# Optimization experiments

Measured on AMD Instinct MI355X. Metric: run time of the kernel, lower is better.

The kernel has to match this reference:

```python
import jax, jax.numpy as jnp
import numpy as np

M = 8192          # tokens (batch*seq)
K = 4096          # in_features
N = 4096          # out_features
BK = 64           # block_k (row_block of B)
BN = 64           # block_n (col_block of B)
NR = K // BK      # 64 block rows of B
NC = N // BN      # 64 block cols of B
OCC = 4           # nonzero blocks per column (and per row)
TB = NR * OCC     # total nonzero blocks = 256


def _build_indices():
    # Regular block mask: each column has OCC nonzero block-rows, each row has OCC
    # nonzero block-cols (matches BlockMask.regular invariants). Deterministic
    # construction: column c uses rows (c + s*(NR//OCC)) % NR, sorted ascending.
    step = NR // OCC
    cols = np.arange(NC)
    rows = np.sort((cols[None, :] + step * np.arange(OCC)[:, None]) % NR, axis=0)  # [OCC, NC]
    # _build_data_indices assigns data slots column-major, row-ascending within a
    # column, so column c's blocks (sorted by row) get slots c*OCC + s.
    data = cols[None, :] * OCC + np.arange(OCC)[:, None]  # [OCC, NC]
    return rows.astype(np.int32), data.astype(np.int32)


def setup_inputs() -> dict:
    key = jax.random.key(0)
    k1, k2 = jax.random.split(key)
    rows, data = _build_indices()
    return {
        "A": jax.random.normal(k1, (M, K), dtype=jnp.float32),
        "B_data": jax.random.normal(k2, (BK, BN * TB), dtype=jnp.float32) * 0.02,
        "row_indices": jnp.asarray(rows),
        "data_indices": jnp.asarray(data),
    }


def reference(A, B_data, row_indices, data_indices):
    # A: [M, K]; B_data: [BK, BN*TB]; indices: [OCC, NC]
    m, k = A.shape
    occ, nc = row_indices.shape
    bk = B_data.shape[0]
    tb = occ * nc
    bn = B_data.shape[1] // tb
    nr = k // bk
    # Gather A blocks per (sub_k, out_col): [m, occ, nc, bk]
    A_blocks = A.reshape(m, nr, bk)[:, row_indices]
    # Gather B blocks: B_data laid out as [bk, tb, bn] -> [tb, bk, bn] -> [occ, nc, bk, bn]
    B_blocks = jnp.transpose(B_data.reshape(bk, tb, bn), (1, 0, 2))[data_indices]
    # Accumulate over occ and bk (fp32 accumulation like the Triton kernel)
    C = jnp.einsum('mock,ockn->mcn', A_blocks, B_blocks,
                   preferred_element_type=jnp.float32)
    return C.reshape(m, nc * bn).astype(A.dtype)
```

## Files before the change

### kernel.cpp

```cpp
#include <hip/hip_runtime.h>
#include <hip/hip_bf16.h>

typedef __bf16 bf16x8 __attribute__((ext_vector_type(8)));
typedef float  f32x4  __attribute__((ext_vector_type(4)));

__device__ __forceinline__ void dma16(const float* g, float* l) {
    typedef const __attribute__((address_space(1))) unsigned int* gp_t;
    typedef __attribute__((address_space(3))) unsigned int*       lp_t;
    __builtin_amdgcn_global_load_lds((gp_t)(const void*)g, (lp_t)(void*)l, 16, 0, 0);
}

__global__ __launch_bounds__(256, 2) void sparse_linear_kernel(
    const float* __restrict__ A, const float* __restrict__ Bd,
    const int* __restrict__ rowi, const int* __restrict__ di,
    float* __restrict__ C)
{
    __shared__ __align__(16) unsigned short Bt[4 * 64 * 64];
    __shared__ __align__(16) float Aring[4][3][16 * 64];
    char* BtB = (char*)Bt;

    const int bid = blockIdx.x;
    const int c   = bid & 63;
    const int mch = bid >> 6;
    const int t    = threadIdx.x;
    const int lane = t & 63;
    const int w    = t >> 6;

    int rs[4], ds[4];
    #pragma unroll
    for (int s = 0; s < 4; ++s) {
        rs[s] = rowi[s * 64 + c];
        ds[s] = di[s * 64 + c];
    }
    int koff[4];
    #pragma unroll
    for (int s = 0; s < 4; ++s) koff[s] = rs[s] * 64;

    const long mbase = (long)mch * 256 + w * 64;

    #pragma unroll
    for (int st = 0; st < 3; ++st) {
        float* slotp = &Aring[w][st][0];
        #pragma unroll
        for (int i = 0; i < 4; ++i) {
            const int rr  = i * 4 + (lane >> 4);
            const int kfl = (((lane & 15) * 16) ^ (rr << 4)) >> 2;
            const float* g = A + (mbase + st * 16 + rr) * 4096 + koff[0] + kfl;
            dma16(g, slotp + i * 256);
        }
    }

    {
        const int n  = t & 63;
        const int sb = t >> 6;
        const float* Bg = Bd + (long)ds[sb] * 64 + n;
        char* dst = BtB + sb * 8192 + n * 128;
        const int sw = (n & 7) << 4;
        #pragma unroll
        for (int k4 = 0; k4 < 16; ++k4) {
            union { ushort4 u; __bf16 e[4]; } pk;
            pk.e[0] = (__bf16)Bg[(long)(4 * k4 + 0) * 16384];
            pk.e[1] = (__bf16)Bg[(long)(4 * k4 + 1) * 16384];
            pk.e[2] = (__bf16)Bg[(long)(4 * k4 + 2) * 16384];
            pk.e[3] = (__bf16)Bg[(long)(4 * k4 + 3) * 16384];
            *(ushort4*)(dst + ((8 * k4) ^ sw)) = pk.u;
        }
    }
    __syncthreads();

    f32x4 acc[4][4];
    #pragma unroll
    for (int m = 0; m < 4; ++m)
        #pragma unroll
        for (int n2 = 0; n2 < 4; ++n2) acc[m][n2] = f32x4{0.f, 0.f, 0.f, 0.f};

    bf16x8 bfr[2][4];

    #pragma unroll
    for (int step = 0; step < 16; ++step) {
        const int s = step >> 2, mt = step & 3, slot = step % 3;

        if (step <= 13)      asm volatile("s_waitcnt vmcnt(8)" ::: "memory");
        else if (step == 14) asm volatile("s_waitcnt vmcnt(4)" ::: "memory");
        else                 asm volatile("s_waitcnt vmcnt(0)" ::: "memory");
        __builtin_amdgcn_sched_barrier(0);

        if (mt == 0) {
            const char* bbase = BtB + s * 8192;
            #pragma unroll
            for (int kh = 0; kh < 2; ++kh)
                #pragma unroll
                for (int n2 = 0; n2 < 4; ++n2) {
                    const int nr = n2 * 16 + (lane & 15);
                    const int kb = kh * 64 + (lane >> 4) * 16;
                    bfr[kh][n2] = *(const bf16x8*)(bbase + nr * 128 + (kb ^ ((nr & 7) << 4)));
                }
        }

        const char* ab = (const char*)&Aring[w][slot][0];
        const int r   = lane & 15;
        const int q32 = (lane >> 4) * 32;
        f32x4 a0 = *(const f32x4*)(ab + r * 256 + ((q32)            ^ (r << 4)));
        f32x4 a1 = *(const f32x4*)(ab + r * 256 + ((q32 + 16)       ^ (r << 4)));
        f32x4 a2 = *(const f32x4*)(ab + r * 256 + ((128 + q32)      ^ (r << 4)));
        f32x4 a3 = *(const f32x4*)(ab + r * 256 + ((128 + q32 + 16) ^ (r << 4)));
        union { bf16x8 v; __bf16 e[8]; } af0, af1;
        #pragma unroll
        for (int i = 0; i < 4; ++i) {
            af0.e[i]     = (__bf16)a0[i];
            af0.e[i + 4] = (__bf16)a1[i];
            af1.e[i]     = (__bf16)a2[i];
            af1.e[i + 4] = (__bf16)a3[i];
        }

        __builtin_amdgcn_s_setprio(1);
        #pragma unroll
        for (int kh = 0; kh < 2; ++kh) {
            const bf16x8 afv = kh ? af1.v : af0.v;
            #pragma unroll
            for (int n2 = 0; n2 < 4; ++n2)
                acc[mt][n2] = __builtin_amdgcn_mfma_f32_16x16x32_bf16(afv, bfr[kh][n2], acc[mt][n2], 0, 0, 0);
        }
        __builtin_amdgcn_s_setprio(0);

        if (step + 3 < 16) {
            const int s2 = (step + 3) >> 2, mt2 = (step + 3) & 3;
            float* slotp = &Aring[w][slot][0];
            #pragma unroll
            for (int i = 0; i < 4; ++i) {
                const int rr  = i * 4 + (lane >> 4);
                const int kfl = (((lane & 15) * 16) ^ (rr << 4)) >> 2;
                const float* g = A + (mbase + mt2 * 16 + rr) * 4096 + koff[s2] + kfl;
                dma16(g, slotp + i * 256);
            }
        }
    }

    #pragma unroll
    for (int mt = 0; mt < 4; ++mt) {
        const long crow0 = mbase + mt * 16 + (lane >> 4) * 4;
        const long col0  = (long)c * 64 + (lane & 15);
        #pragma unroll
        for (int n2 = 0; n2 < 4; ++n2)
            #pragma unroll
            for (int v = 0; v < 4; ++v)
                __builtin_nontemporal_store(acc[mt][n2][v],
                    &C[(crow0 + v) * 4096 + col0 + n2 * 16]);
    }
}

extern "C" void kernel_launch(void* const* d_in, const int* in_sizes, int n_in,
                              void* d_out, int out_size, void* d_ws, size_t ws_size,
                              hipStream_t stream) {
    const float* A    = (const float*)d_in[0];
    const float* Bd   = (const float*)d_in[1];
    const int*   rowi = (const int*)d_in[2];
    const int*   di   = (const int*)d_in[3];
    float*       C    = (float*)d_out;

    dim3 grid(32 * 64);
    dim3 block(256);
    hipLaunchKernelGGL(sparse_linear_kernel, grid, block, 0, stream,
                       A, Bd, rowi, di, C);
}
```

Baseline: 58.45 us.

## Process four M-chunks per block to reuse converted B tile, quarter grid

Each workgroup now handles four 256-row chunks of A for its output column block instead of one, so the B-block gather and bf16 conversion into LDS is amortised over four times more work and the grid shrinks from 2048 to 512 blocks. The A DMA ring runs continuously across chunk boundaries, and each chunk's results are written out and the accumulators reset before the next chunk begins. With 256 CUs and 2 blocks/CU this leaves exactly one wave of blocks, but it removes the tail-overlap benefit of more blocks. Store traffic issued mid-loop may interfere with the vmcnt-based waits. The final chunk also issues redundant clamped prefetches.

Measured after the change: 56.25 us. 3.8% less time.

```diff
diff --git a/kernel.cpp b/kernel.cpp
--- a/kernel.cpp
+++ b/kernel.cpp
@@ -15,13 +15,13 @@
     const int* __restrict__ rowi, const int* __restrict__ di,
     float* __restrict__ C)
 {
+    __shared__ __align__(16) float Aring[4][3][16 * 64];
     __shared__ __align__(16) unsigned short Bt[4 * 64 * 64];
-    __shared__ __align__(16) float Aring[4][3][16 * 64];
     char* BtB = (char*)Bt;
 
     const int bid = blockIdx.x;
     const int c   = bid & 63;
-    const int mch = bid >> 6;
+    const int grp = bid >> 6;
     const int t    = threadIdx.x;
     const int lane = t & 63;
     const int w    = t >> 6;
@@ -36,19 +36,22 @@
     #pragma unroll
     for (int s = 0; s < 4; ++s) koff[s] = rs[s] * 64;
 
-    const long mbase = (long)mch * 256 + w * 64;
+    const long wrow0 = (long)grp * 1024 + w * 64;
 
-    #pragma unroll
-    for (int st = 0; st < 3; ++st) {
-        float* slotp = &Aring[w][st][0];
+    auto dmaA = [&](int q, int kb, int mt, int slot) {
+        float* slotp = &Aring[w][slot][0];
         #pragma unroll
         for (int i = 0; i < 4; ++i) {
             const int rr  = i * 4 + (lane >> 4);
             const int kfl = (((lane & 15) * 16) ^ (rr << 4)) >> 2;
-            const float* g = A + (mbase + st * 16 + rr) * 4096 + koff[0] + kfl;
+            const float* g = A + (wrow0 + q * 256 + mt * 16 + rr) * 4096 + koff[kb] + kfl;
             dma16(g, slotp + i * 256);
         }
-    }
+    };
+
+    dmaA(0, 0, 0, 0);
+    dmaA(0, 0, 1, 1);
+    dmaA(0, 0, 2, 2);
 
     {
         const int n  = t & 63;
@@ -58,12 +61,12 @@
         const int sw = (n & 7) << 4;
         #pragma unroll
         for (int k4 = 0; k4 < 16; ++k4) {
-            union { ushort4 u; __bf16 e[4]; } pk;
+            union { ushort4 u4; __bf16 e[4]; } pk;
             pk.e[0] = (__bf16)Bg[(long)(4 * k4 + 0) * 16384];
             pk.e[1] = (__bf16)Bg[(long)(4 * k4 + 1) * 16384];
             pk.e[2] = (__bf16)Bg[(long)(4 * k4 + 2) * 16384];
             pk.e[3] = (__bf16)Bg[(long)(4 * k4 + 3) * 16384];
-            *(ushort4*)(dst + ((8 * k4) ^ sw)) = pk.u;
+            *(ushort4*)(dst + ((8 * k4) ^ sw)) = pk.u4;
         }
     }
     __syncthreads();
@@ -76,77 +79,86 @@
 
     bf16x8 bfr[2][4];
 
-    #pragma unroll
-    for (int step = 0; step < 16; ++step) {
-        const int s = step >> 2, mt = step & 3, slot = step % 3;
+    #pragma unroll 1
+    for (int q = 0; q < 4; ++q) {
+        const int qm3 = q % 3;
 
-        if (step <= 13)      asm volatile("s_waitcnt vmcnt(8)" ::: "memory");
-        else if (step == 14) asm volatile("s_waitcnt vmcnt(4)" ::: "memory");
-        else                 asm volatile("s_waitcnt vmcnt(0)" ::: "memory");
-        __builtin_amdgcn_sched_barrier(0);
+        #pragma unroll
+        for (int local = 0; local < 16; ++local) {
+            const int kb = local >> 2, mt = local & 3;
+            int slot = qm3 + (local % 3);
+            if (slot >= 3) slot -= 3;
 
-        if (mt == 0) {
-            const char* bbase = BtB + s * 8192;
-            #pragma unroll
-            for (int kh = 0; kh < 2; ++kh)
+            if (local < 3) asm volatile("s_waitcnt vmcnt(24)" ::: "memory");
+            else           asm volatile("s_waitcnt vmcnt(8)"  ::: "memory");
+            __builtin_amdgcn_sched_barrier(0);
+
+            if (mt == 0) {
+                const char* bbase = BtB + kb * 8192;
                 #pragma unroll
-                for (int n2 = 0; n2 < 4; ++n2) {
-                    const int nr = n2 * 16 + (lane & 15);
-                    const int kb = kh * 64 + (lane >> 4) * 16;
-                    bfr[kh][n2] = *(const bf16x8*)(bbase + nr * 128 + (kb ^ ((nr & 7) << 4)));
-                }
-        }
+                for (int kh = 0; kh < 2; ++kh)
+                    #pragma unroll
+                    for (int n2 = 0; n2 < 4; ++n2) {
+                        const int nr = n2 * 16 + (lane & 15);
+                        const int kbyte = kh * 64 + (lane >> 4) * 16;
+                        bfr[kh][n2] = *(const bf16x8*)(bbase + nr * 128 + (kbyte ^ ((nr & 7) << 4)));
+                    }
+            }
 
-        const char* ab = (const char*)&Aring[w][slot][0];
-        const int r   = lane & 15;
-        const int q32 = (lane >> 4) * 32;
-        f32x4 a0 = *(const f32x4*)(ab + r * 256 + ((q32)            ^ (r << 4)));
-        f32x4 a1 = *(const f32x4*)(ab + r * 256 + ((q32 + 16)       ^ (r << 4)));
-        f32x4 a2 = *(const f32x4*)(ab + r * 256 + ((128 + q32)      ^ (r << 4)));
-        f32x4 a3 = *(const f32x4*)(ab + r * 256 + ((128 + q32 + 16) ^ (r << 4)));
-        union { bf16x8 v; __bf16 e[8]; } af0, af1;
-        #pragma unroll
-        for (int i = 0; i < 4; ++i) {
-            af0.e[i]     = (__bf16)a0[i];
-            af0.e[i + 4] = (__bf16)a1[i];
-            af1.e[i]     = (__bf16)a2[i];
-            af1.e[i + 4] = (__bf16)a3[i];
-        }
-
-        __builtin_amdgcn_s_setprio(1);
-        #pragma unroll
-        for (int kh = 0; kh < 2; ++kh) {
-            const bf16x8 afv = kh ? af1.v : af0.v;
-            #pragma unroll
-            for (int n2 = 0; n2 < 4; ++n2)
-                acc[mt][n2] = __builtin_amdgcn_mfma_f32_16x16x32_bf16(afv, bfr[kh][n2], acc[mt][n2], 0, 0, 0);
-        }
-        __builtin_amdgcn_s_setprio(0);
-
-        if (step + 3 < 16) {
-            const int s2 = (step + 3) >> 2, mt2 = (step + 3) & 3;
-            float* slotp = &Aring[w][slot][0];
+            const char* ab = (const char*)&Aring[w][slot][0];
+            const int r   = lane & 15;
+            const int q32 = (lane >> 4) * 32;
+            f32x4 a0 = *(const f32x4*)(ab + r * 256 + ((q32)            ^ (r << 4)));
+            f32x4 a1 = *(const f32x4*)(ab + r * 256 + ((q32 + 16)       ^ (r << 4)));
+            f32x4 a2 = *(const f32x4*)(ab + r * 256 + ((128 + q32)      ^ (r << 4)));
+            f32x4 a3 = *(const f32x4*)(ab + r * 256 + ((128 + q32 + 16) ^ (r << 4)));
+            union { bf16x8 v; __bf16 e[8]; } af0, af1;
             #pragma unroll
             for (int i = 0; i < 4; ++i) {
-                const int rr  = i * 4 + (lane >> 4);
-                const int kfl = (((lane & 15) * 16) ^ (rr << 4)) >> 2;
-                const float* g = A + (mbase + mt2 * 16 + rr) * 4096 + koff[s2] + kfl;
-                dma16(g, slotp + i * 256);
+                af0.e[i]     = (__bf16)a0[i];
+                af0.e[i + 4] = (__bf16)a1[i];
+                af1.e[i]     = (__bf16)a2[i];
+                af1.e[i + 4] = (__bf16)a3[i];
+            }
+
+            __builtin_amdgcn_s_setprio(1);
+            #pragma unroll
+            for (int kh = 0; kh < 2; ++kh) {
+                const bf16x8 afv = kh ? af1.v : af0.v;
+                #pragma unroll
+                for (int n2 = 0; n2 < 4; ++n2)
+                    acc[mt][n2] = __builtin_amdgcn_mfma_f32_16x16x32_bf16(afv, bfr[kh][n2], acc[mt][n2], 0, 0, 0);
+            }
+            __builtin_amdgcn_s_setprio(0);
+
+            {
+                int l2 = local + 3, q2 = q;
+                if (l2 >= 16) { l2 -= 16; ++q2; }
+                if (q2 > 3) q2 = 3;
+                dmaA(q2, l2 >> 2, l2 & 3, slot);
+            }
+
+            if (local == 15) {
+                __builtin_amdgcn_sched_barrier(0);
+                #pragma unroll
+                for (int mts = 0; mts < 4; ++mts) {
+                    const long crow0 = wrow0 + q * 256 + mts * 16 + (lane >> 4) * 4;
+                    const long col0  = (long)c * 64 + (lane & 15);
+                    #pragma unroll
+                    for (int n2 = 0; n2 < 4; ++n2) {
+                        #pragma unroll
+                        for (int v = 0; v < 4; ++v)
+                            __builtin_nontemporal_store(acc[mts][n2][v],
+                                &C[(crow0 + v) * 4096 + col0 + n2 * 16]);
+                        acc[mts][n2] = f32x4{0.f, 0.f, 0.f, 0.f};
+                    }
+                }
+                __builtin_amdgcn_sched_barrier(0);
             }
         }
     }
 
-    #pragma unroll
-    for (int mt = 0; mt < 4; ++mt) {
-        const long crow0 = mbase + mt * 16 + (lane >> 4) * 4;
-        const long col0  = (long)c * 64 + (lane & 15);
-        #pragma unroll
-        for (int n2 = 0; n2 < 4; ++n2)
-            #pragma unroll
-            for (int v = 0; v < 4; ++v)
-                __builtin_nontemporal_store(acc[mt][n2][v],
-                    &C[(crow0 + v) * 4096 + col0 + n2 * 16]);
-    }
+    asm volatile("s_waitcnt vmcnt(0)" ::: "memory");
 }
 
 extern "C" void kernel_launch(void* const* d_in, const int* in_sizes, int n_in,
@@ -158,7 +170,7 @@
     const int*   di   = (const int*)d_in[3];
     float*       C    = (float*)d_out;
 
-    dim3 grid(32 * 64);
+    dim3 grid(8 * 64);
     dim3 block(256);
     hipLaunchKernelGGL(sparse_linear_kernel, grid, block, 0, stream,
                        A, Bd, rowi, di, C);
```
